# Kernel optimization log

Measured on AMD Instinct MI355X. Metric: run time of the kernel, lower is better.

## Reference

```python
import jax, jax.numpy as jnp
from jax import lax
import numpy as np

RPN_BBOX_STD_DEV = np.array([0.1, 0.1, 0.2, 0.2], dtype=np.float32)
PRE_NMS_LIMIT = 2048      # anchors kept before NMS (sorted by score)
NUM_PROPOSAL = 1000       # post-NMS proposal count (init kwarg num_proposal)
NMS_THRESHOLD = 0.7       # init kwarg nms_threshold


def setup_inputs() -> dict:
    key = jax.random.key(0)
    k1, k2, k3, k4, k5, k6 = jax.random.split(key, 6)
    B, N = 4, 1_000_000
    rpn_probs = jax.random.uniform(k1, (B, N, 2), dtype=jnp.float32)
    rpn_bbox = jax.random.normal(k2, (B, N, 4), dtype=jnp.float32)
    # well-formed normalized anchors (y1, x1, y2, x2)
    cy = jax.random.uniform(k3, (B, N), dtype=jnp.float32)
    cx = jax.random.uniform(k4, (B, N), dtype=jnp.float32)
    h = jax.random.uniform(k5, (B, N), dtype=jnp.float32) * 0.25 + 0.05
    w = jax.random.uniform(k6, (B, N), dtype=jnp.float32) * 0.25 + 0.05
    anchors = jnp.stack([cy - 0.5 * h, cx - 0.5 * w, cy + 0.5 * h, cx + 0.5 * w], axis=-1)
    return {"rpn_probs": rpn_probs, "rpn_bbox": rpn_bbox, "anchors": anchors}


def apply_box_deltas(boxes, deltas):
    # boxes: (..., 4) as (y1, x1, y2, x2); deltas: (dy, dx, log(dh), log(dw))
    h = boxes[..., 2] - boxes[..., 0]
    w = boxes[..., 3] - boxes[..., 1]
    cy = boxes[..., 0] + 0.5 * h + deltas[..., 0] * h
    cx = boxes[..., 1] + 0.5 * w + deltas[..., 1] * w
    h = h * jnp.exp(deltas[..., 2])
    w = w * jnp.exp(deltas[..., 3])
    return jnp.stack([cy - 0.5 * h, cx - 0.5 * w, cy + 0.5 * h, cx + 0.5 * w], axis=-1)


def pairwise_iou(boxes):
    # boxes: (P, 4) -> (P, P)
    y1, x1, y2, x2 = boxes[:, 0], boxes[:, 1], boxes[:, 2], boxes[:, 3]
    area = (y2 - y1) * (x2 - x1)
    ih = jnp.maximum(jnp.minimum(y2[:, None], y2[None, :]) - jnp.maximum(y1[:, None], y1[None, :]), 0.0)
    iw = jnp.maximum(jnp.minimum(x2[:, None], x2[None, :]) - jnp.maximum(x1[:, None], x1[None, :]), 0.0)
    inter = ih * iw
    union = area[:, None] + area[None, :] - inter
    return inter / (union + 1e-8)


def nms_single(boxes):
    # boxes (P, 4) sorted by score desc; greedy NMS then pad/clip to NUM_PROPOSAL
    P = boxes.shape[0]
    iou = pairwise_iou(boxes)
    idx = jnp.arange(P)

    def body(keep, i):
        suppress = keep[i] & (iou[i] > NMS_THRESHOLD) & (idx > i)
        return keep & ~suppress, None

    keep, _ = lax.scan(body, jnp.ones((P,), jnp.bool_), idx)
    rank = jnp.cumsum(keep) - 1                      # position among kept boxes
    valid = keep & (rank < NUM_PROPOSAL)
    pos = jnp.where(valid, rank, NUM_PROPOSAL)       # overflow row dropped below
    out = jnp.zeros((NUM_PROPOSAL + 1, 4), boxes.dtype).at[pos].set(
        jnp.where(valid[:, None], boxes, 0.0))
    return out[:NUM_PROPOSAL]


def reference(rpn_probs, rpn_bbox, anchors):
    scores = rpn_probs[:, :, 1]                                  # foreground prob (B, N)
    deltas = rpn_bbox * jnp.asarray(RPN_BBOX_STD_DEV)
    _, ix = lax.top_k(scores, PRE_NMS_LIMIT)                     # (B, P)
    deltas_top = jnp.take_along_axis(deltas, ix[..., None], axis=1)
    anchors_top = jnp.take_along_axis(anchors, ix[..., None], axis=1)
    boxes = apply_box_deltas(anchors_top, deltas_top)            # (B, P, 4)
    boxes = jnp.clip(boxes, 0.0, 1.0)                            # clip to [0,1] window
    proposals = jax.vmap(nms_single)(boxes)                      # (B, NUM_PROPOSAL, 4)
    return proposals
```

## Files before the change

kernel.cpp:

```cpp
#include <hip/hip_runtime.h>

#define B_ 4
#define N_ 1000000
#define K_ 2048
#define P_ 1000
#define CAP_ 8192
#define THR_ 0.7f
#define NF4_ 500000
#define META_STRIDE 32
#define TILE_ 512
#define NCH_ (CAP_ / TILE_)

#define OFF_HIST 0
#define OFF_META 1048576
#define OFF_COARSE (OFF_META + 1024)
#define OFF_CAND (OFF_COARSE + 4096)
#define OFF_TOPI (OFF_CAND + 262144)
#define OFF_BOX  (OFF_TOPI + 32768)
#define OFF_MASK (OFF_BOX + 131072)

__device__ __forceinline__ unsigned fkey(float f) {
  unsigned u = __float_as_uint(f);
  return (u & 0x80000000u) ? ~u : (u | 0x80000000u);
}

__device__ __forceinline__ unsigned long long readlane64(unsigned long long v, int l) {
  unsigned lo = (unsigned)__builtin_amdgcn_readlane((int)(unsigned)(v & 0xffffffffull), l);
  unsigned hi = (unsigned)__builtin_amdgcn_readlane((int)(unsigned)(v >> 32), l);
  return ((unsigned long long)hi << 32) | (unsigned long long)lo;
}

#define PIN16(k) asm volatile("" : "+v"(k[0]), "+v"(k[1]), "+v"(k[2]), "+v"(k[3]), \
                                   "+v"(k[4]), "+v"(k[5]), "+v"(k[6]), "+v"(k[7]), \
                                   "+v"(k[8]), "+v"(k[9]), "+v"(k[10]), "+v"(k[11]), \
                                   "+v"(k[12]), "+v"(k[13]), "+v"(k[14]), "+v"(k[15]))

__global__ void __launch_bounds__(1024) hist_kernel(const float4* __restrict__ probs4,
                                                    unsigned* __restrict__ hist) {
  int b = blockIdx.y;
  __shared__ unsigned h[32768];
  for (int i = threadIdx.x; i < 32768; i += 1024) h[i] = 0u;
  __syncthreads();
  const float4* p4 = probs4 + (size_t)b * NF4_;
  int base = blockIdx.x * 8192;
  float4 v[8];
#pragma unroll
  for (int c = 0; c < 8; ++c) {
    int i4 = base + c * 1024 + threadIdx.x;
    v[c] = (i4 < NF4_) ? p4[i4] : make_float4(0.f, 0.f, 0.f, 0.f);
  }
  unsigned k[16];
#pragma unroll
  for (int c = 0; c < 8; ++c) { k[2 * c] = fkey(v[c].y) >> 16; k[2 * c + 1] = fkey(v[c].w) >> 16; }
  PIN16(k);
#pragma unroll
  for (int c = 0; c < 8; ++c) {
    int i4 = base + c * 1024 + threadIdx.x;
    if (i4 < NF4_) {
      unsigned b0 = k[2 * c], b1 = k[2 * c + 1];
      atomicAdd(&h[b0 >> 1], 1u << ((b0 & 1u) << 4));
      atomicAdd(&h[b1 >> 1], 1u << ((b1 & 1u) << 4));
    }
  }
  __syncthreads();
  unsigned* g = hist + ((size_t)b << 16);
  for (int w = threadIdx.x; w < 32768; w += 1024) {
    unsigned x = h[w];
    if (x) {
      unsigned c0 = x & 0xFFFFu, c1 = x >> 16;
      if (c0) atomicAdd(&g[2 * w], c0);
      if (c1) atomicAdd(&g[2 * w + 1], c1);
    }
  }
}

__global__ void __launch_bounds__(64) coarse_kernel(const unsigned* __restrict__ hist,
                                                    unsigned* __restrict__ coarse) {
  int b = blockIdx.y, g = blockIdx.x, lane = threadIdx.x;
  const uint4* h4 = (const uint4*)(hist + (((size_t)b) << 16) + ((size_t)g << 8));
  uint4 v = h4[lane];
  unsigned s = v.x + v.y + v.z + v.w;
#pragma unroll
  for (int off = 32; off >= 1; off >>= 1) s += __shfl_xor(s, off, 64);
  if (lane == 0) coarse[b * 256 + g] = s;
}

__global__ void select_kernel(const unsigned* __restrict__ hist, const unsigned* __restrict__ coarse,
                              unsigned* __restrict__ meta) {
  int b = blockIdx.x, t = threadIdx.x;
  __shared__ unsigned suf[256];
  __shared__ int tc_s;
  __shared__ unsigned above_s;
  const unsigned* g = hist + ((size_t)b << 16);
  suf[t] = coarse[b * 256 + t];
  __syncthreads();
  for (int off = 1; off < 256; off <<= 1) {
    unsigned add = (t + off < 256) ? suf[t + off] : 0u;
    __syncthreads();
    suf[t] += add;
    __syncthreads();
  }
  unsigned nxt = (t < 255) ? suf[t + 1] : 0u;
  if (suf[t] >= K_ && (t == 255 || nxt < K_)) { tc_s = t; above_s = nxt; }
  __syncthreads();
  int tc = tc_s;
  unsigned above = above_s;
  unsigned bs = g[tc * 256 + t];
  __syncthreads();
  suf[t] = bs;
  __syncthreads();
  for (int off = 1; off < 256; off <<= 1) {
    unsigned add = (t + off < 256) ? suf[t + off] : 0u;
    __syncthreads();
    suf[t] += add;
    __syncthreads();
  }
  unsigned nxt2 = (t < 255) ? suf[t + 1] : 0u;
  if (above + suf[t] >= K_ && (t == 255 || above + nxt2 < K_))
    meta[b * META_STRIDE + 0] = (unsigned)(tc * 256 + t);
}

__global__ void __launch_bounds__(256) compact_kernel(const float4* __restrict__ probs4,
                                                      unsigned* __restrict__ meta,
                                                      uint2* __restrict__ cand) {
  int b = blockIdx.y;
  __shared__ unsigned lcnt, gbase_s;
  __shared__ uint2 buf[4096];
  if (threadIdx.x == 0) lcnt = 0u;
  __syncthreads();
  unsigned cb = meta[b * META_STRIDE + 0];
  const float4* p4 = probs4 + (size_t)b * NF4_;
  int base = blockIdx.x * 2048;
  int lane = threadIdx.x & 63;
  float4 v[8];
#pragma unroll
  for (int c = 0; c < 8; ++c) {
    int i4 = base + c * 256 + threadIdx.x;
    v[c] = (i4 < NF4_) ? p4[i4] : make_float4(0.f, 0.f, 0.f, 0.f);
  }
  unsigned k[16];
#pragma unroll
  for (int c = 0; c < 8; ++c) { k[2 * c] = fkey(v[c].y); k[2 * c + 1] = fkey(v[c].w); }
  PIN16(k);
#pragma unroll
  for (int c = 0; c < 8; ++c) {
#pragma unroll
    for (int s = 0; s < 2; ++s) {
      int i4 = base + c * 256 + threadIdx.x;
      unsigned key = k[2 * c + s];
      bool pass = (i4 < NF4_) && ((key >> 16) >= cb);
      unsigned long long m = __ballot(pass);
      if (m) {
        int leader = __ffsll(m) - 1;
        unsigned wbase = 0;
        if (lane == leader) wbase = atomicAdd(&lcnt, (unsigned)__popcll(m));
        wbase = __shfl(wbase, leader, 64);
        if (pass) {
          unsigned pos = wbase + (unsigned)__popcll(m & ((1ull << lane) - 1ull));
          buf[pos] = make_uint2(key, (unsigned)(2 * i4 + s));
        }
      }
    }
  }
  __syncthreads();
  unsigned cnt = lcnt;
  if (threadIdx.x == 0) gbase_s = atomicAdd(&meta[b * META_STRIDE + 1], cnt);
  __syncthreads();
  unsigned gbase = gbase_s;
  for (unsigned i = threadIdx.x; i < cnt; i += 256) {
    unsigned pos = gbase + i;
    if (pos < CAP_) cand[(size_t)b * CAP_ + pos] = buf[i];
  }
}

__global__ void __launch_bounds__(256) rank_kernel(const uint2* __restrict__ cand,
                                                   const unsigned* __restrict__ meta,
                                                   unsigned* __restrict__ partial) {
  int b = blockIdx.z;
  unsigned M = meta[b * META_STRIDE + 1];
  if (M > CAP_) M = CAP_;
  unsigned tb = blockIdx.y * TILE_;
  if (tb >= M) return;
  if ((unsigned)(blockIdx.x * 256) >= M) return;
  __shared__ __align__(16) uint2 tile[TILE_];
  unsigned n = M - tb;
  if (n > TILE_) n = TILE_;
  for (unsigned t = threadIdx.x; t < n; t += 256) tile[t] = cand[(size_t)b * CAP_ + tb + t];
  int ci = blockIdx.x * 256 + threadIdx.x;
  bool act = ci < (int)M;
  uint2 me = make_uint2(0u, 0u);
  if (act) me = cand[(size_t)b * CAP_ + ci];
  unsigned long long my = ((unsigned long long)me.x << 32) | (unsigned long long)(unsigned)(~me.y);
  __syncthreads();
  if (act) {
    unsigned rank = 0;
    unsigned n2 = n >> 1;
    const uint4* t4 = (const uint4*)tile;
    for (unsigned j = 0; j < n2; ++j) {
      uint4 v = t4[j];
      unsigned long long c0 = ((unsigned long long)v.x << 32) | (unsigned long long)(unsigned)(~v.y);
      unsigned long long c1 = ((unsigned long long)v.z << 32) | (unsigned long long)(unsigned)(~v.w);
      rank += (unsigned)(c0 > my) + (unsigned)(c1 > my);
    }
    if (n & 1) {
      uint2 v = tile[n - 1];
      unsigned long long c0 = ((unsigned long long)v.x << 32) | (unsigned long long)(unsigned)(~v.y);
      rank += (unsigned)(c0 > my);
    }
    partial[((size_t)b * NCH_ + blockIdx.y) * CAP_ + ci] = rank;
  }
}

__global__ void __launch_bounds__(256) scatter_kernel(const uint2* __restrict__ cand,
                                                      const unsigned* __restrict__ meta,
                                                      const unsigned* __restrict__ partial,
                                                      const float4* __restrict__ bbox,
                                                      const float4* __restrict__ anch,
                                                      float4* __restrict__ boxes) {
  int b = blockIdx.y;
  unsigned M = meta[b * META_STRIDE + 1];
  if (M > CAP_) M = CAP_;
  unsigned ci = blockIdx.x * 256 + threadIdx.x;
  if (ci >= M) return;
  unsigned nch = (M + TILE_ - 1) / TILE_;
  const unsigned* pp = partial + (size_t)b * NCH_ * CAP_ + ci;
  unsigned rank = 0;
  for (unsigned c = 0; c < nch; ++c) rank += pp[(size_t)c * CAP_];
  if (rank >= K_) return;
  unsigned idx = cand[(size_t)b * CAP_ + ci].y;
  size_t base = (size_t)b * N_ + idx;
  float4 a = anch[base];
  float4 d = bbox[base];
  float d0 = d.x * 0.1f, d1 = d.y * 0.1f, d2 = d.z * 0.2f, d3 = d.w * 0.2f;
  float h = a.z - a.x, w = a.w - a.y;
  float cy = (a.x + 0.5f * h) + d0 * h;
  float cx = (a.y + 0.5f * w) + d1 * w;
  float h2 = h * expf(d2);
  float w2 = w * expf(d3);
  float y1 = cy - 0.5f * h2, x1 = cx - 0.5f * w2;
  float y2 = cy + 0.5f * h2, x2 = cx + 0.5f * w2;
  y1 = fminf(fmaxf(y1, 0.f), 1.f);
  x1 = fminf(fmaxf(x1, 0.f), 1.f);
  y2 = fminf(fmaxf(y2, 0.f), 1.f);
  x2 = fminf(fmaxf(x2, 0.f), 1.f);
  boxes[(b << 11) + rank] = make_float4(y1, x1, y2, x2);
}

__global__ void mask_kernel(const float4* __restrict__ boxes, unsigned long long* __restrict__ mask) {
  int wid = blockIdx.x * 4 + (threadIdx.x >> 6);
  int lane = threadIdx.x & 63;
  int b = wid >> 12;
  int rb = (wid >> 5) & 127;
  int jb = wid & 31;
  if (jb < (rb >> 2)) return;
  int j = (jb << 6) + lane;
  float4 bj = boxes[(b << 11) + j];
  float areaJ = (bj.z - bj.x) * (bj.w - bj.y);
#pragma unroll
  for (int r = 0; r < 16; ++r) {
    int i = (rb << 4) + r;
    float4 bi = boxes[(b << 11) + i];
    float areaI = (bi.z - bi.x) * (bi.w - bi.y);
    float yA = fmaxf(bi.x, bj.x), xA = fmaxf(bi.y, bj.y);
    float yB = fminf(bi.z, bj.z), xB = fminf(bi.w, bj.w);
    float ih = fmaxf(yB - yA, 0.f), iw = fmaxf(xB - xA, 0.f);
    float inter = ih * iw;
    float uni = areaI + areaJ - inter;
    float iou = inter / (uni + 1e-8f);
    bool pred = (iou > THR_) && (j > i);
    unsigned long long bits = __ballot(pred);
    if (lane == 0) mask[((size_t)((b << 11) + i) << 5) + jb] = bits;
  }
}

__global__ void __launch_bounds__(256) nms_kernel(const unsigned long long* __restrict__ mask,
                                                  const float4* __restrict__ boxes,
                                                  float4* __restrict__ out) {
  int b = blockIdx.x;
  int t = threadIdx.x;
  int wid = t >> 6, lane = t & 63;
  int w = lane & 31, half = lane >> 5;
  __shared__ unsigned long long rows[2][64][33];
  __shared__ unsigned long long remS[32];
  __shared__ unsigned long long keptm[32];
  __shared__ int pre[32];
  __shared__ short sel[P_];
  __shared__ int stopF;
  if (t < 32) { remS[t] = 0ull; keptm[t] = 0ull; }
  if (t == 0) stopF = 0;
  for (int r = t; r < P_; r += 256) sel[r] = -1;
  const unsigned long long* mbase = mask + (((size_t)(b << 11)) << 5);
  unsigned long long r0[8];
  int rowb = 2 * wid + half;
#pragma unroll
  for (int j = 0; j < 8; ++j) r0[j] = mbase[j * 256 + t];
#pragma unroll
  for (int j = 0; j < 8; ++j) rows[0][8 * j + rowb][w] = r0[j];
  __syncthreads();
  int cb = 0;
  int cnt = 0;
  for (int c = 0; c < 32; ++c) {
    bool pf = (c < 31) && (w > c);
    if (pf) {
      const unsigned long long* srcN = mbase + (((size_t)(c + 1)) << 11);
#pragma unroll
      for (int j = 0; j < 8; ++j) r0[j] = srcN[j * 256 + t];
    }
    if (wid == 0) {
      unsigned long long rin = rows[cb][lane][c];
      unsigned long long cur = remS[c];
      unsigned long long bm = __ballot(rin != 0ull);
      while (bm) {
        int k2 = __ffsll((long long)bm) - 1;
        bm &= bm - 1;
        if (!((cur >> k2) & 1ull)) cur |= readlane64(rin, k2);
      }
      unsigned long long kept = ~cur;
      cnt += (int)__popcll(kept);
      if (lane == 0) {
        keptm[c] = kept;
        if (cnt >= P_) stopF = 1;
      }
    }
    __syncthreads();
    if (stopF) break;
    if (w > c) {
      unsigned long long kept = keptm[c];
      unsigned long long acc = 0ull;
#pragma unroll
      for (int j = 0; j < 8; ++j) {
        int row = 8 * j + rowb;
        acc |= rows[cb][row][w] & (0ull - ((kept >> row) & 1ull));
      }
      acc |= __shfl_xor(acc, 32, 64);
      if (half == 0) {
        unsigned lo = (unsigned)acc, hi = (unsigned)(acc >> 32);
        unsigned* rp = (unsigned*)&remS[w];
        if (lo) atomicOr(rp, lo);
        if (hi) atomicOr(rp + 1, hi);
      }
    }
    if (pf) {
#pragma unroll
      for (int j = 0; j < 8; ++j) rows[cb ^ 1][8 * j + rowb][w] = r0[j];
    }
    __syncthreads();
    cb ^= 1;
  }
  __syncthreads();
  if (t == 0) {
    int run = 0;
    for (int c = 0; c < 32; ++c) { pre[c] = run; run += (int)__popcll(keptm[c]); }
  }
  __syncthreads();
  for (int i = t; i < K_; i += 256) {
    int c = i >> 6, k2 = i & 63;
    unsigned long long km = keptm[c];
    if ((km >> k2) & 1ull) {
      int rank = pre[c] + (int)__popcll(km & ((1ull << k2) - 1ull));
      if (rank < P_) sel[rank] = (short)i;
    }
  }
  __syncthreads();
  for (int r = t; r < P_; r += 256) {
    int i = sel[r];
    float4 v = make_float4(0.f, 0.f, 0.f, 0.f);
    if (i >= 0) v = boxes[(b << 11) + i];
    out[b * P_ + r] = v;
  }
}

extern "C" void kernel_launch(void* const* d_in, const int* in_sizes, int n_in,
                              void* d_out, int out_size, void* d_ws, size_t ws_size,
                              hipStream_t stream) {
  const float4* probs4 = (const float4*)d_in[0];
  const float4* bbox   = (const float4*)d_in[1];
  const float4* anch   = (const float4*)d_in[2];
  char* ws = (char*)d_ws;
  unsigned* hist = (unsigned*)(ws + OFF_HIST);
  unsigned* meta = (unsigned*)(ws + OFF_META);
  unsigned* coarse = (unsigned*)(ws + OFF_COARSE);
  uint2* cand = (uint2*)(ws + OFF_CAND);
  float4* boxes = (float4*)(ws + OFF_BOX);
  unsigned long long* mask = (unsigned long long*)(ws + OFF_MASK);
  unsigned* partial = (unsigned*)(ws + OFF_MASK);
  float4* out = (float4*)d_out;

  hipMemsetAsync(ws, 0, OFF_COARSE, stream);

  hist_kernel<<<dim3(62, B_), 1024, 0, stream>>>(probs4, hist);
  coarse_kernel<<<dim3(256, B_), 64, 0, stream>>>(hist, coarse);
  select_kernel<<<B_, 256, 0, stream>>>(hist, coarse, meta);
  compact_kernel<<<dim3(245, B_), 256, 0, stream>>>(probs4, meta, cand);
  rank_kernel<<<dim3(CAP_ / 256, NCH_, B_), 256, 0, stream>>>(cand, meta, partial);
  scatter_kernel<<<dim3(CAP_ / 256, B_), 256, 0, stream>>>(cand, meta, partial, bbox, anch, boxes);
  mask_kernel<<<(B_ * 128 * 32) / 4, 256, 0, stream>>>(boxes, mask);
  nms_kernel<<<B_, 256, 0, stream>>>(mask, boxes, out);
}
```

Before: 218.3 us.

## Replace sequential chunked NMS with sparse fixed-point iteration over nonzero mask rows

The mask kernel now records, per box row, whether that row suppresses anything, using an atomic bitmap. The NMS kernel compacts those rows into an event list and stages up to 448 of them in shared memory. It then finds the greedy suppression set by parallel fixed-point iteration: each pass ORs together the rows of boxes that are not currently suppressed, and passes repeat until the set stops changing. The first 1536 rows are solved first, with an early exit once at least 1000 boxes are kept. This removes the 32-step serial walk with its per-step barriers, at the cost of adding atomics to the mask kernel and an iteration count that depends on suppression chain depth.

```diff
diff --git a/kernel.cpp b/kernel.cpp
--- a/kernel.cpp
+++ b/kernel.cpp
@@ -10,14 +10,16 @@
 #define META_STRIDE 32
 #define TILE_ 512
 #define NCH_ (CAP_ / TILE_)
+#define NSTAGE 448
+#define CROW 1536
 
 #define OFF_HIST 0
 #define OFF_META 1048576
-#define OFF_COARSE (OFF_META + 1024)
-#define OFF_CAND (OFF_COARSE + 4096)
-#define OFF_TOPI (OFF_CAND + 262144)
-#define OFF_BOX  (OFF_TOPI + 32768)
-#define OFF_MASK (OFF_BOX + 131072)
+#define OFF_COARSE 1049600
+#define OFF_ROWANY 1053696
+#define OFF_CAND 1054720
+#define OFF_BOX  1316864
+#define OFF_MASK 1447936
 
 __device__ __forceinline__ unsigned fkey(float f) {
   unsigned u = __float_as_uint(f);
@@ -246,7 +248,8 @@
   boxes[(b << 11) + rank] = make_float4(y1, x1, y2, x2);
 }
 
-__global__ void mask_kernel(const float4* __restrict__ boxes, unsigned long long* __restrict__ mask) {
+__global__ void mask_kernel(const float4* __restrict__ boxes, unsigned long long* __restrict__ mask,
+                            unsigned long long* __restrict__ rowAny) {
   int wid = blockIdx.x * 4 + (threadIdx.x >> 6);
   int lane = threadIdx.x & 63;
   int b = wid >> 12;
@@ -269,93 +272,114 @@
     float iou = inter / (uni + 1e-8f);
     bool pred = (iou > THR_) && (j > i);
     unsigned long long bits = __ballot(pred);
-    if (lane == 0) mask[((size_t)((b << 11) + i) << 5) + jb] = bits;
+    if (lane == 0) {
+      mask[((size_t)((b << 11) + i) << 5) + jb] = bits;
+      if (bits) atomicOr(&rowAny[b * 32 + (i >> 6)], 1ull << (i & 63));
+    }
   }
 }
 
 __global__ void __launch_bounds__(256) nms_kernel(const unsigned long long* __restrict__ mask,
+                                                  const unsigned long long* __restrict__ rowAny,
                                                   const float4* __restrict__ boxes,
                                                   float4* __restrict__ out) {
   int b = blockIdx.x;
   int t = threadIdx.x;
-  int wid = t >> 6, lane = t & 63;
-  int w = lane & 31, half = lane >> 5;
-  __shared__ unsigned long long rows[2][64][33];
-  __shared__ unsigned long long remS[32];
-  __shared__ unsigned long long keptm[32];
+  int w = t & 31, g = t >> 5;
+  __shared__ unsigned long long rowsBuf[NSTAGE][32];
+  __shared__ unsigned short evRow[2048];
+  __shared__ unsigned long long supA[32], supB[32];
   __shared__ int pre[32];
   __shared__ short sel[P_];
-  __shared__ int stopF;
-  if (t < 32) { remS[t] = 0ull; keptm[t] = 0ull; }
-  if (t == 0) stopF = 0;
+  __shared__ int E_s, EC_s, chg_s, cnt_s;
   for (int r = t; r < P_; r += 256) sel[r] = -1;
-  const unsigned long long* mbase = mask + (((size_t)(b << 11)) << 5);
-  unsigned long long r0[8];
-  int rowb = 2 * wid + half;
-#pragma unroll
-  for (int j = 0; j < 8; ++j) r0[j] = mbase[j * 256 + t];
-#pragma unroll
-  for (int j = 0; j < 8; ++j) rows[0][8 * j + rowb][w] = r0[j];
-  __syncthreads();
-  int cb = 0;
-  int cnt = 0;
-  for (int c = 0; c < 32; ++c) {
-    bool pf = (c < 31) && (w > c);
-    if (pf) {
-      const unsigned long long* srcN = mbase + (((size_t)(c + 1)) << 11);
-#pragma unroll
-      for (int j = 0; j < 8; ++j) r0[j] = srcN[j * 256 + t];
-    }
-    if (wid == 0) {
-      unsigned long long rin = rows[cb][lane][c];
-      unsigned long long cur = remS[c];
-      unsigned long long bm = __ballot(rin != 0ull);
+  if (t < 32) { supA[t] = 0ull; supB[t] = 0ull; }
+  if (t == 0) { E_s = 0; EC_s = 0; chg_s = 0; }
+  if (t < 64) {
+    unsigned long long anyv = (t < 32) ? rowAny[b * 32 + t] : 0ull;
+    unsigned pc = (unsigned)__popcll(anyv);
+    unsigned pref = pc;
+#pragma unroll
+    for (int off = 1; off < 32; off <<= 1) {
+      unsigned tv = __shfl_up(pref, off, 64);
+      if ((t & 31) >= off) pref += tv;
+    }
+    if (t == 31) E_s = (int)pref;
+    if (t == 23) EC_s = (int)pref;
+    if (t < 32) {
+      unsigned o = pref - pc;
+      unsigned long long bm = anyv;
       while (bm) {
-        int k2 = __ffsll((long long)bm) - 1;
+        int i = __ffsll((long long)bm) - 1;
         bm &= bm - 1;
-        if (!((cur >> k2) & 1ull)) cur |= readlane64(rin, k2);
+        evRow[o++] = (unsigned short)((t << 6) + i);
       }
-      unsigned long long kept = ~cur;
-      cnt += (int)__popcll(kept);
-      if (lane == 0) {
-        keptm[c] = kept;
-        if (cnt >= P_) stopF = 1;
+    }
+  }
+  __syncthreads();
+  int E = E_s, EC = EC_s;
+  const unsigned long long* mb = mask + (((size_t)(b << 11)) << 5);
+  int ns = (E < NSTAGE) ? E : NSTAGE;
+  for (int base = 0; base < ns; base += 64) {
+    unsigned long long v[8];
+#pragma unroll
+    for (int j = 0; j < 8; ++j) {
+      int e = base + j * 8 + g;
+      v[j] = 0ull;
+      if (e < ns) {
+        int r = (int)evRow[e];
+        if (w >= (r >> 6)) v[j] = mb[((size_t)r << 5) + w];
       }
     }
-    __syncthreads();
-    if (stopF) break;
-    if (w > c) {
-      unsigned long long kept = keptm[c];
-      unsigned long long acc = 0ull;
-#pragma unroll
-      for (int j = 0; j < 8; ++j) {
-        int row = 8 * j + rowb;
-        acc |= rows[cb][row][w] & (0ull - ((kept >> row) & 1ull));
+#pragma unroll
+    for (int j = 0; j < 8; ++j) {
+      int e = base + j * 8 + g;
+      if (e < ns) rowsBuf[e][w] = v[j];
+    }
+  }
+  __syncthreads();
+  unsigned long long* cur = supA;
+  unsigned long long* nxt = supB;
+  int limit = EC;
+  for (;;) {
+    unsigned long long acc = 0ull;
+    for (int e = g; e < limit; e += 8) {
+      int r = (int)evRow[e];
+      int rw = r >> 6;
+      if (w >= rw) {
+        unsigned long long sw = cur[rw];
+        if (!((sw >> (r & 63)) & 1ull))
+          acc |= (e < NSTAGE) ? rowsBuf[e][w] : mb[((size_t)r << 5) + w];
       }
-      acc |= __shfl_xor(acc, 32, 64);
-      if (half == 0) {
-        unsigned lo = (unsigned)acc, hi = (unsigned)(acc >> 32);
-        unsigned* rp = (unsigned*)&remS[w];
-        if (lo) atomicOr(rp, lo);
-        if (hi) atomicOr(rp + 1, hi);
-      }
-    }
-    if (pf) {
-#pragma unroll
-      for (int j = 0; j < 8; ++j) rows[cb ^ 1][8 * j + rowb][w] = r0[j];
-    }
-    __syncthreads();
-    cb ^= 1;
-  }
-  __syncthreads();
+    }
+    if (acc) atomicOr((unsigned long long*)&nxt[w], acc);
+    __syncthreads();
+    if (t < 32) {
+      if (t == 0) chg_s = 0;
+      if (nxt[t] != cur[t]) chg_s = 1;
+      cur[t] = 0ull;
+    }
+    __syncthreads();
+    { unsigned long long* tmp = cur; cur = nxt; nxt = tmp; }
+    if (chg_s) continue;
+    if (limit >= E) break;
+    if (t == 0) {
+      int c = 0;
+      for (int i = 0; i < 24; ++i) c += (int)__popcll(cur[i]);
+      cnt_s = CROW - c;
+    }
+    __syncthreads();
+    if (cnt_s >= P_) break;
+    limit = E;
+  }
   if (t == 0) {
     int run = 0;
-    for (int c = 0; c < 32; ++c) { pre[c] = run; run += (int)__popcll(keptm[c]); }
+    for (int c = 0; c < 32; ++c) { pre[c] = run; run += (int)__popcll(~cur[c]); }
   }
   __syncthreads();
   for (int i = t; i < K_; i += 256) {
     int c = i >> 6, k2 = i & 63;
-    unsigned long long km = keptm[c];
+    unsigned long long km = ~cur[c];
     if ((km >> k2) & 1ull) {
       int rank = pre[c] + (int)__popcll(km & ((1ull << k2) - 1ull));
       if (rank < P_) sel[rank] = (short)i;
@@ -380,13 +404,14 @@
   unsigned* hist = (unsigned*)(ws + OFF_HIST);
   unsigned* meta = (unsigned*)(ws + OFF_META);
   unsigned* coarse = (unsigned*)(ws + OFF_COARSE);
+  unsigned long long* rowAny = (unsigned long long*)(ws + OFF_ROWANY);
   uint2* cand = (uint2*)(ws + OFF_CAND);
   float4* boxes = (float4*)(ws + OFF_BOX);
   unsigned long long* mask = (unsigned long long*)(ws + OFF_MASK);
   unsigned* partial = (unsigned*)(ws + OFF_MASK);
   float4* out = (float4*)d_out;
 
-  hipMemsetAsync(ws, 0, OFF_COARSE, stream);
+  hipMemsetAsync(ws, 0, OFF_CAND, stream);
 
   hist_kernel<<<dim3(62, B_), 1024, 0, stream>>>(probs4, hist);
   coarse_kernel<<<dim3(256, B_), 64, 0, stream>>>(hist, coarse);
@@ -394,6 +419,6 @@
   compact_kernel<<<dim3(245, B_), 256, 0, stream>>>(probs4, meta, cand);
   rank_kernel<<<dim3(CAP_ / 256, NCH_, B_), 256, 0, stream>>>(cand, meta, partial);
   scatter_kernel<<<dim3(CAP_ / 256, B_), 256, 0, stream>>>(cand, meta, partial, bbox, anch, boxes);
-  mask_kernel<<<(B_ * 128 * 32) / 4, 256, 0, stream>>>(boxes, mask);
-  nms_kernel<<<B_, 256, 0, stream>>>(mask, boxes, out);
-}
+  mask_kernel<<<(B_ * 128 * 32) / 4, 256, 0, stream>>>(boxes, mask, rowAny);
+  nms_kernel<<<B_, 256, 0, stream>>>(mask, rowAny, boxes, out);
+}
```

New measurement: 250.8 us. +14.9%, slower.
